# Optimization experiments

Hardware: AMD Instinct MI355X
Metric: run time of the kernel (lower is better)

Reference implementation:

```python
import jax, jax.numpy as jnp
import numpy as np

BZ, C, H, W = 8, 512, 64, 64


def setup_inputs() -> dict:
    key = jax.random.key(0)
    x = jax.random.normal(key, (BZ, C, H, W), dtype=jnp.float32)
    # central square hole: flag==1 -> masked (unknown), flag==0 -> known
    mask = np.zeros((H, W), dtype=np.int32)
    mask[H // 4: 3 * H // 4, W // 4: 3 * W // 4] = 1
    return {"x": x, "mask": jnp.asarray(mask)}


def reference(x, mask):
    # InnerShiftSingle forward with shift_sz=1, stride=1, mask_thred=1:
    # flag == feature-level mask (each 1x1 patch is masked iff its pixel is masked).
    bz, c, h, w = x.shape
    c2 = c // 2
    hw = h * w
    flag = mask.reshape(hw)  # [hw] int, 1=masked, 0=known

    former = x[:, :c2]   # decoder features [b,c2,h,w]
    latter = x[:, c2:]   # encoder features [b,c2,h,w]

    former_f = former.reshape(bz, c2, hw).transpose(0, 2, 1)  # [b,hw,c2]
    latter_f = latter.reshape(bz, c2, hw).transpose(0, 2, 1)  # [b,hw,c2]

    # original: conv of (un-normalized) former with L2-normalized latter 1x1 patches
    latter_n = latter_f / (jnp.linalg.norm(latter_f, axis=-1, keepdims=True) + 1e-8)
    cosine = jnp.einsum('bpc,bqc->bpq', former_f, latter_n)  # [b,hw,hw]
    # only known-region patches (flag==0) are candidate sources
    cosine = jnp.where(flag[None, None, :] == 1, -jnp.inf, cosine)

    best = jnp.argmax(cosine, axis=-1)  # [b,hw] index into known region
    shift = jnp.take_along_axis(latter_f, best[..., None], axis=1)  # [b,hw,c2]
    # only masked positions receive a shifted feature; known positions stay 0
    shift = jnp.where(flag[None, :, None] == 1, shift, jnp.zeros((), x.dtype))
    shift = shift.transpose(0, 2, 1).reshape(bz, c2, h, w)

    return jnp.concatenate([former, latter, shift], axis=1)  # [b, 3c/2, h, w]
```

## Files before the change

### kernel.cpp

```cpp
#include <hip/hip_runtime.h>
#include <math.h>

#define BZc 8
#define Cc 512
#define C2c 256
#define HWc 4096
#define OUTC 768
#define NP 1024
#define NQ 3072
#define QG 8
#define TAU 5e-5f
#define FIXSLOTS 64

typedef _Float16 h8 __attribute__((ext_vector_type(8)));
typedef float f16v __attribute__((ext_vector_type(16)));
typedef float f32x4 __attribute__((ext_vector_type(4)));

__global__ __launch_bounds__(1024) void k_build(const int* __restrict__ mask,
                                                int* __restrict__ pidx,
                                                int* __restrict__ qidx,
                                                int* __restrict__ qinv,
                                                int* __restrict__ cnt) {
    __shared__ int s0[1024], s1[1024], t0[1024], t1[1024];
    int t = threadIdx.x;
    if (t < 8) cnt[t] = 0;
    int f[4];
    int cp = 0;
#pragma unroll
    for (int j = 0; j < 4; ++j) { f[j] = mask[t * 4 + j]; cp += f[j]; }
    s0[t] = cp; s1[t] = 4 - cp;
    __syncthreads();
    int *a = s0, *b = s1, *c = t0, *d = t1;
    for (int off = 1; off < 1024; off <<= 1) {
        int vp = a[t] + (t >= off ? a[t - off] : 0);
        int vq = b[t] + (t >= off ? b[t - off] : 0);
        c[t] = vp; d[t] = vq;
        __syncthreads();
        int* tmp;
        tmp = a; a = c; c = tmp;
        tmp = b; b = d; d = tmp;
    }
    int ep = a[t] - cp;
    int eq = b[t] - (4 - cp);
#pragma unroll
    for (int j = 0; j < 4; ++j) {
        int idx = t * 4 + j;
        if (f[j]) { pidx[ep] = idx; qinv[idx] = -1; ep++; }
        else      { qidx[eq] = idx; qinv[idx] = eq; eq++; }
    }
}

__global__ __launch_bounds__(256) void k_prep(const float* __restrict__ x,
                                              const int* __restrict__ pidx,
                                              const int* __restrict__ qinv,
                                              _Float16* __restrict__ latH,
                                              _Float16* __restrict__ latL,
                                              _Float16* __restrict__ forH,
                                              _Float16* __restrict__ forL,
                                              float* __restrict__ invn,
                                              float* __restrict__ nrm) {
    int id = blockIdx.x;
    bool isLat = id < 512;
    int b  = isLat ? (id >> 6) : ((id - 512) >> 4);
    int bx = isLat ? (id & 63) : ((id - 512) & 15);
    int tid = threadIdx.x;
    __shared__ float tile[64][65];
    __shared__ float sqa[4][64];
    __shared__ float sinv[64];
    __shared__ int rowm[64];
    __shared__ int rowsrc[64];
    if (tid < 64) {
        if (isLat) { int q = bx * 64 + tid; rowsrc[tid] = q; rowm[tid] = qinv[q]; }
        else       { int pc = bx * 64 + tid; rowsrc[tid] = pidx[pc]; rowm[tid] = pc; }
    }
    __syncthreads();
    const float* xb = x + (size_t)b * Cc * HWc + (isLat ? (size_t)C2c * HWc : 0);
    if (isLat) {
        float sacc = 0.f;
        for (int c0 = 0; c0 < 256; c0 += 64) {
            for (int it = 0; it < 16; ++it) {
                int i = tid + it * 256; int cc = i >> 6, qq = i & 63;
                float v = xb[(size_t)(c0 + cc) * HWc + rowsrc[qq]];
                sacc += v * v;
            }
        }
        sqa[tid >> 6][tid & 63] = sacc;
        __syncthreads();
        if (tid < 64) {
            float s = sqa[0][tid] + sqa[1][tid] + sqa[2][tid] + sqa[3][tid];
            float nr = sqrtf(s) + 1e-8f;
            float inv = 1.0f / nr;
            int q = bx * 64 + tid;
            invn[b * HWc + q] = inv; nrm[b * HWc + q] = nr;
            sinv[tid] = inv;
        }
        __syncthreads();
    }
    _Float16* dH = isLat ? latH + (size_t)b * NQ * 256 : forH + (size_t)b * NP * 256;
    _Float16* dL = isLat ? latL + (size_t)b * NQ * 256 : forL + (size_t)b * NP * 256;
    for (int c0 = 0; c0 < 256; c0 += 64) {
        for (int it = 0; it < 16; ++it) {
            int i = tid + it * 256; int cc = i >> 6, qq = i & 63;
            tile[qq][cc] = xb[(size_t)(c0 + cc) * HWc + rowsrc[qq]];
        }
        __syncthreads();
        int qq = tid >> 2, sub = tid & 3;
        int dr = rowm[qq];
        if (dr >= 0) {
            float scale = isLat ? sinv[qq] : 1.0f;
            h8 hv0, hv1, lv0, lv1;
#pragma unroll
            for (int j = 0; j < 8; ++j) {
                float v = tile[qq][sub * 16 + j] * scale;
                _Float16 h = (_Float16)v;
                hv0[j] = h; lv0[j] = (_Float16)((v - (float)h) * 2048.0f);
            }
#pragma unroll
            for (int j = 0; j < 8; ++j) {
                float v = tile[qq][sub * 16 + 8 + j] * scale;
                _Float16 h = (_Float16)v;
                hv1[j] = h; lv1[j] = (_Float16)((v - (float)h) * 2048.0f);
            }
            size_t o = (size_t)dr * 256 + c0 + sub * 16;
            *(h8*)(dH + o) = hv0; *(h8*)(dH + o + 8) = hv1;
            *(h8*)(dL + o) = lv0; *(h8*)(dL + o + 8) = lv1;
        }
        __syncthreads();
    }
}

__global__ __launch_bounds__(512, 2) void k_gemm(const _Float16* __restrict__ latH,
                                                 const _Float16* __restrict__ latL,
                                                 const _Float16* __restrict__ forH,
                                                 const _Float16* __restrict__ forL,
                                                 float* __restrict__ bv1,
                                                 int* __restrict__ bi1,
                                                 float* __restrict__ bv2) {
    int pg = blockIdx.x;
    int qg = blockIdx.y;
    int b  = blockIdx.z;
    int tid = threadIdx.x;
    int w = tid >> 6, lane = tid & 63;
    int l31 = lane & 31, lh = lane >> 5;

    __shared__ __align__(16) _Float16 sH[2][32 * 256];
    __shared__ __align__(16) _Float16 sL[2][32 * 256];

    size_t fo = ((size_t)(b * NP + pg * 256 + w * 32 + l31)) * 256 + lh * 8;
    const _Float16* fH = forH + fo;
    const _Float16* fL = forL + fo;
    h8 BH[16], BL[16];
#pragma unroll
    for (int ks = 0; ks < 16; ++ks) {
        BH[ks] = *(const h8*)(fH + ks * 16);
        BL[ks] = *(const h8*)(fL + ks * 16);
    }

    const _Float16* latHb = latH + (size_t)(b * NQ + qg * 384) * 256;
    const _Float16* latLb = latL + (size_t)(b * NQ + qg * 384) * 256;
    int sq0 = tid >> 5;
    int sq1 = 16 + (tid >> 5);
    int ssl = tid & 31;

    float v1 = -INFINITY, v2 = -INFINITY; int i1 = 0;

    f32x4 rH0, rH1, rL0, rL1;
#define LOADQ(t)                                                                   \
    rH0 = *(const f32x4*)(latHb + ((size_t)((t) * 32 + sq0) * 256 + ssl * 8));     \
    rH1 = *(const f32x4*)(latHb + ((size_t)((t) * 32 + sq1) * 256 + ssl * 8));     \
    rL0 = *(const f32x4*)(latLb + ((size_t)((t) * 32 + sq0) * 256 + ssl * 8));     \
    rL1 = *(const f32x4*)(latLb + ((size_t)((t) * 32 + sq1) * 256 + ssl * 8));
#define WRITEQ(bf)                                                                 \
    *(f32x4*)(&sH[bf][sq0 * 256 + ((ssl ^ sq0) * 8)]) = rH0;                       \
    *(f32x4*)(&sH[bf][sq1 * 256 + ((ssl ^ sq1) * 8)]) = rH1;                       \
    *(f32x4*)(&sL[bf][sq0 * 256 + ((ssl ^ sq0) * 8)]) = rL0;                       \
    *(f32x4*)(&sL[bf][sq1 * 256 + ((ssl ^ sq1) * 8)]) = rL1;

    LOADQ(0); WRITEQ(0);
    __syncthreads();

    for (int t = 0; t < 12; ++t) {
        if (t < 11) { LOADQ(t + 1); }
        const _Float16* bufH = &sH[t & 1][0];
        const _Float16* bufL = &sL[t & 1][0];
        f16v accA = {}, accB = {};
#pragma unroll
        for (int ks = 0; ks < 16; ++ks) {
            int slotA = (ks * 2 + lh) ^ l31;
            h8 aH = *(const h8*)(bufH + l31 * 256 + slotA * 8);
            h8 aL = *(const h8*)(bufL + l31 * 256 + slotA * 8);
            accA = __builtin_amdgcn_mfma_f32_32x32x16_f16(aH, BH[ks], accA, 0, 0, 0);
            accB = __builtin_amdgcn_mfma_f32_32x32x16_f16(aH, BL[ks], accB, 0, 0, 0);
            accB = __builtin_amdgcn_mfma_f32_32x32x16_f16(aL, BH[ks], accB, 0, 0, 0);
        }
        int q0 = qg * 384 + t * 32;
#pragma unroll
        for (int r = 0; r < 16; ++r) {
            float v = accA[r] + accB[r] * (1.0f / 2048.0f);
            int q = q0 + (r & 3) + 8 * (r >> 2) + 4 * lh;
            if (v > v1) { v2 = v1; v1 = v; i1 = q; }
            else if (v > v2) { v2 = v; }
        }
        if (t < 11) { WRITEQ((t + 1) & 1); }
        __syncthreads();
    }
#undef LOADQ
#undef WRITEQ
    float ov1 = __shfl_xor(v1, 32);
    int   oi1 = __shfl_xor(i1, 32);
    float ov2 = __shfl_xor(v2, 32);
    if (ov1 > v1) { v2 = fmaxf(v1, ov2); v1 = ov1; i1 = oi1; }
    else          { v2 = fmaxf(ov1, v2); }
    if (lane < 32) {
        size_t o = ((size_t)b * NP + pg * 256 + w * 32 + lane) * QG + qg;
        bv1[o] = v1; bi1[o] = i1; bv2[o] = v2;
    }
}

__global__ void k_reduce(const float* __restrict__ bv1, const int* __restrict__ bi1,
                         const float* __restrict__ bv2, int* __restrict__ bfin,
                         int* __restrict__ cnt, int* __restrict__ fixrows) {
    int t = blockIdx.x * blockDim.x + threadIdx.x;
    if (t >= BZc * NP) return;
    float V1 = -INFINITY, V2 = -INFINITY; int I1 = 0;
    for (int c = 0; c < QG; ++c) {
        float a = bv1[(size_t)t * QG + c];
        float a2 = bv2[(size_t)t * QG + c];
        int   i = bi1[(size_t)t * QG + c];
        if (a > V1) { V2 = fmaxf(V1, a2); V1 = a; I1 = i; }
        else        { V2 = fmaxf(V2, a); }
    }
    bfin[t] = I1;
    if (V1 - V2 < TAU) {
        int b = t >> 10;
        int s = atomicAdd(&cnt[b], 1);
        if (s < FIXSLOTS) fixrows[b * FIXSLOTS + s] = t & 1023;
    }
}

__global__ __launch_bounds__(256) void k_fixA(const float* __restrict__ x,
                                              const int* __restrict__ pidx,
                                              const int* __restrict__ mask,
                                              const float* __restrict__ invn,
                                              const int* __restrict__ cnt,
                                              const int* __restrict__ fixrows,
                                              float* __restrict__ fixv,
                                              int* __restrict__ fixi) {
    int qg = blockIdx.x, s = blockIdx.y, b = blockIdx.z;
    int n = cnt[b]; if (n > FIXSLOTS) n = FIXSLOTS;
    if (s >= n) return;
    int p = fixrows[b * FIXSLOTS + s];
    int porig = pidx[p];
    int tid = threadIdx.x;
    __shared__ float fs[256];
    fs[tid] = x[((size_t)b * Cc + tid) * HWc + porig];
    __syncthreads();
    const float* lx = x + ((size_t)b * Cc + C2c) * HWc;
    int q0 = qg * 1024 + tid * 4;
    float4 acc = make_float4(0.f, 0.f, 0.f, 0.f);
    for (int c0 = 0; c0 < 256; c0 += 8) {
        float4 v[8];
#pragma unroll
        for (int u = 0; u < 8; ++u)
            v[u] = *(const float4*)(lx + (size_t)(c0 + u) * HWc + q0);
#pragma unroll
        for (int u = 0; u < 8; ++u) {
            float fc = fs[c0 + u];
            acc.x = fmaf(fc, v[u].x, acc.x);
            acc.y = fmaf(fc, v[u].y, acc.y);
            acc.z = fmaf(fc, v[u].z, acc.z);
            acc.w = fmaf(fc, v[u].w, acc.w);
        }
    }
    float vals[4] = {acc.x, acc.y, acc.z, acc.w};
    float bv = -INFINITY; int bq = 1 << 30;
#pragma unroll
    for (int k = 0; k < 4; ++k) {
        int q = q0 + k;
        float val = vals[k] * invn[b * HWc + q];
        if (mask[q] == 0 && val > bv) { bv = val; bq = q; }
    }
    __shared__ float rv[256]; __shared__ int rq[256];
    rv[tid] = bv; rq[tid] = bq; __syncthreads();
    for (int off = 128; off > 0; off >>= 1) {
        if (tid < off) {
            float v2 = rv[tid + off]; int q2 = rq[tid + off];
            if (v2 > rv[tid] || (v2 == rv[tid] && q2 < rq[tid])) { rv[tid] = v2; rq[tid] = q2; }
        }
        __syncthreads();
    }
    if (tid == 0) {
        fixv[(b * FIXSLOTS + s) * 4 + qg] = rv[0];
        fixi[(b * FIXSLOTS + s) * 4 + qg] = rq[0];
    }
}

__global__ void k_fixB(const int* __restrict__ cnt, const int* __restrict__ fixrows,
                       const float* __restrict__ fixv, const int* __restrict__ fixi,
                       const int* __restrict__ qinv, int* __restrict__ bfin) {
    int t = threadIdx.x;
    int b = t >> 6, s = t & 63;
    int n = cnt[b]; if (n > FIXSLOTS) n = FIXSLOTS;
    if (s >= n) return;
    float bv = -INFINITY; int bq = 1 << 30;
    for (int qg = 0; qg < 4; ++qg) {
        float v = fixv[(b * FIXSLOTS + s) * 4 + qg];
        int   q = fixi[(b * FIXSLOTS + s) * 4 + qg];
        if (v > bv || (v == bv && q < bq)) { bv = v; bq = q; }
    }
    int p = fixrows[b * FIXSLOTS + s];
    bfin[b * NP + p] = qinv[bq];
}

__global__ __launch_bounds__(256) void k_fill(const float* __restrict__ x,
                                              float* __restrict__ out) {
    size_t i4 = (size_t)blockIdx.x * blockDim.x + threadIdx.x;
    size_t total4 = (size_t)BZc * OUTC * HWc / 4;
    if (i4 >= total4) return;
    size_t e   = i4 * 4;
    size_t per = (size_t)OUTC * HWc;
    size_t b   = e / per;
    size_t rem = e % per;
    int ch = (int)(rem / HWc);
    float4* o4 = (float4*)out;
    if (ch < Cc) {
        const float4* x4 = (const float4*)x;
        o4[i4] = x4[((size_t)b * Cc * HWc + rem) >> 2];
    } else {
        o4[i4] = make_float4(0.f, 0.f, 0.f, 0.f);
    }
}

__global__ __launch_bounds__(256) void k_scatter(const _Float16* __restrict__ latH,
                                                 const _Float16* __restrict__ latL,
                                                 const float* __restrict__ nrm,
                                                 const int* __restrict__ bfin,
                                                 const int* __restrict__ pidx,
                                                 const int* __restrict__ qidx,
                                                 float* __restrict__ out) {
    int blk = blockIdx.x;
    int b   = blockIdx.y;
    int tid = threadIdx.x;
    __shared__ float tile[32][257];
    __shared__ int qd[32], pd[32];
    __shared__ float nr[32];
    if (tid < 32) {
        int qc = bfin[b * NP + blk * 32 + tid];
        qd[tid] = qc;
        pd[tid] = pidx[blk * 32 + tid];
        nr[tid] = nrm[b * HWc + qidx[qc]];
    }
    __syncthreads();
    for (int i = tid; i < 32 * 256; i += 256) {
        int pp = i >> 8, c = i & 255;
        size_t o = ((size_t)b * NQ + qd[pp]) * 256 + c;
        tile[pp][c] = ((float)latH[o] + (float)latL[o] * (1.0f / 2048.0f)) * nr[pp];
    }
    __syncthreads();
    float* ob = out + (size_t)b * OUTC * HWc + (size_t)Cc * HWc;
    for (int i = tid; i < 256 * 32; i += 256) {
        int ch = i >> 5, j = i & 31;
        ob[(size_t)ch * HWc + pd[j]] = tile[j][ch];
    }
}

extern "C" void kernel_launch(void* const* d_in, const int* in_sizes, int n_in,
                              void* d_out, int out_size, void* d_ws, size_t ws_size,
                              hipStream_t stream) {
    const float* x    = (const float*)d_in[0];
    const int*   mask = (const int*)d_in[1];
    float* out = (float*)d_out;
    char*  ws  = (char*)d_ws;

    _Float16* latH = (_Float16*)(ws);
    _Float16* latL = (_Float16*)(ws + 12582912);
    _Float16* forH = (_Float16*)(ws + 25165824);
    _Float16* forL = (_Float16*)(ws + 29360128);
    float* invn    = (float*)(ws + 33554432);
    float* nrm     = (float*)(ws + 33685504);
    float* bv1     = (float*)(ws + 33816576);
    int*   bi1     = (int*)  (ws + 34078720);
    float* bv2     = (float*)(ws + 34340864);
    int*   bfin    = (int*)  (ws + 34603008);
    int*   pidx    = (int*)  (ws + 34635776);
    int*   qidx    = (int*)  (ws + 34639872);
    int*   qinv    = (int*)  (ws + 34652160);
    int*   cnt     = (int*)  (ws + 34668544);
    int*   fixrows = (int*)  (ws + 34668576);
    float* fixv    = (float*)(ws + 34670624);
    int*   fixi    = (int*)  (ws + 34678816);

    k_build<<<1, 1024, 0, stream>>>(mask, pidx, qidx, qinv, cnt);
    k_prep<<<640, 256, 0, stream>>>(x, pidx, qinv, latH, latL, forH, forL, invn, nrm);
    k_fill<<<(int)(((size_t)BZc * OUTC * HWc / 4 + 255) / 256), 256, 0, stream>>>(x, out);
    k_gemm<<<dim3(4, QG, BZc), 512, 0, stream>>>(latH, latL, forH, forL, bv1, bi1, bv2);
    k_reduce<<<(BZc * NP + 255) / 256, 256, 0, stream>>>(bv1, bi1, bv2, bfin, cnt, fixrows);
    k_fixA<<<dim3(4, FIXSLOTS, BZc), 256, 0, stream>>>(x, pidx, mask, invn, cnt, fixrows, fixv, fixi);
    k_fixB<<<1, 512, 0, stream>>>(cnt, fixrows, fixv, fixi, qinv, bfin);
    k_scatter<<<dim3(32, BZc), 256, 0, stream>>>(latH, latL, nrm, bfin, pidx, qidx, out);
}
```

Measured before the change: 132.2 us.

## Fuse output copy and zero-fill into prep; apply inverse norm in GEMM epilogue

The separate k_fill pass is removed. k_prep now reads x once with contiguous spatial rows, writes the former and latter channels straight to the output, and zeroes the shift channels. Latent features are stored unnormalized, and the per-candidate inverse norm is applied in the GEMM epilogue from shared memory. The scatter therefore no longer rescales by the norm, and the separate norm pass over the latent channels disappears. The trade-off is that prep now runs over all 64-column groups, including masked rows for latent and known rows for former, and it does extra output writes. Precision also shifts slightly, because the fp16 hi/lo split now carries the raw values rather than normalized ones.

```diff
diff --git a/kernel.cpp b/kernel.cpp
--- a/kernel.cpp
+++ b/kernel.cpp
@@ -18,8 +18,8 @@
 
 __global__ __launch_bounds__(1024) void k_build(const int* __restrict__ mask,
                                                 int* __restrict__ pidx,
-                                                int* __restrict__ qidx,
                                                 int* __restrict__ qinv,
+                                                int* __restrict__ pinv,
                                                 int* __restrict__ cnt) {
     __shared__ int s0[1024], s1[1024], t0[1024], t1[1024];
     int t = threadIdx.x;
@@ -45,79 +45,58 @@
 #pragma unroll
     for (int j = 0; j < 4; ++j) {
         int idx = t * 4 + j;
-        if (f[j]) { pidx[ep] = idx; qinv[idx] = -1; ep++; }
-        else      { qidx[eq] = idx; qinv[idx] = eq; eq++; }
+        if (f[j]) { pidx[ep] = idx; pinv[idx] = ep; qinv[idx] = -1; ep++; }
+        else      { qinv[idx] = eq; pinv[idx] = -1; eq++; }
     }
 }
 
 __global__ __launch_bounds__(256) void k_prep(const float* __restrict__ x,
-                                              const int* __restrict__ pidx,
+                                              const int* __restrict__ pinv,
                                               const int* __restrict__ qinv,
                                               _Float16* __restrict__ latH,
                                               _Float16* __restrict__ latL,
                                               _Float16* __restrict__ forH,
                                               _Float16* __restrict__ forL,
                                               float* __restrict__ invn,
-                                              float* __restrict__ nrm) {
+                                              float* __restrict__ invnC,
+                                              float* __restrict__ out) {
     int id = blockIdx.x;
     bool isLat = id < 512;
-    int b  = isLat ? (id >> 6) : ((id - 512) >> 4);
-    int bx = isLat ? (id & 63) : ((id - 512) & 15);
+    int b = isLat ? (id >> 6) : ((id - 512) >> 6);
+    int g = isLat ? (id & 63) : ((id - 512) & 63);
     int tid = threadIdx.x;
     __shared__ float tile[64][65];
     __shared__ float sqa[4][64];
-    __shared__ float sinv[64];
     __shared__ int rowm[64];
-    __shared__ int rowsrc[64];
-    if (tid < 64) {
-        if (isLat) { int q = bx * 64 + tid; rowsrc[tid] = q; rowm[tid] = qinv[q]; }
-        else       { int pc = bx * 64 + tid; rowsrc[tid] = pidx[pc]; rowm[tid] = pc; }
-    }
+    if (tid < 64) rowm[tid] = isLat ? qinv[g * 64 + tid] : pinv[g * 64 + tid];
     __syncthreads();
     const float* xb = x + (size_t)b * Cc * HWc + (isLat ? (size_t)C2c * HWc : 0);
-    if (isLat) {
-        float sacc = 0.f;
-        for (int c0 = 0; c0 < 256; c0 += 64) {
-            for (int it = 0; it < 16; ++it) {
-                int i = tid + it * 256; int cc = i >> 6, qq = i & 63;
-                float v = xb[(size_t)(c0 + cc) * HWc + rowsrc[qq]];
-                sacc += v * v;
-            }
-        }
-        sqa[tid >> 6][tid & 63] = sacc;
-        __syncthreads();
-        if (tid < 64) {
-            float s = sqa[0][tid] + sqa[1][tid] + sqa[2][tid] + sqa[3][tid];
-            float nr = sqrtf(s) + 1e-8f;
-            float inv = 1.0f / nr;
-            int q = bx * 64 + tid;
-            invn[b * HWc + q] = inv; nrm[b * HWc + q] = nr;
-            sinv[tid] = inv;
-        }
-        __syncthreads();
-    }
+    float* ob = out + (size_t)b * OUTC * HWc + (isLat ? (size_t)C2c * HWc : 0);
     _Float16* dH = isLat ? latH + (size_t)b * NQ * 256 : forH + (size_t)b * NP * 256;
     _Float16* dL = isLat ? latL + (size_t)b * NQ * 256 : forL + (size_t)b * NP * 256;
+    float sacc = 0.f;
     for (int c0 = 0; c0 < 256; c0 += 64) {
         for (int it = 0; it < 16; ++it) {
             int i = tid + it * 256; int cc = i >> 6, qq = i & 63;
-            tile[qq][cc] = xb[(size_t)(c0 + cc) * HWc + rowsrc[qq]];
+            float v = xb[(size_t)(c0 + cc) * HWc + g * 64 + qq];
+            tile[qq][cc] = v;
+            ob[(size_t)(c0 + cc) * HWc + g * 64 + qq] = v;
+            sacc += v * v;
         }
         __syncthreads();
         int qq = tid >> 2, sub = tid & 3;
         int dr = rowm[qq];
         if (dr >= 0) {
-            float scale = isLat ? sinv[qq] : 1.0f;
             h8 hv0, hv1, lv0, lv1;
 #pragma unroll
             for (int j = 0; j < 8; ++j) {
-                float v = tile[qq][sub * 16 + j] * scale;
+                float v = tile[qq][sub * 16 + j];
                 _Float16 h = (_Float16)v;
                 hv0[j] = h; lv0[j] = (_Float16)((v - (float)h) * 2048.0f);
             }
 #pragma unroll
             for (int j = 0; j < 8; ++j) {
-                float v = tile[qq][sub * 16 + 8 + j] * scale;
+                float v = tile[qq][sub * 16 + 8 + j];
                 _Float16 h = (_Float16)v;
                 hv1[j] = h; lv1[j] = (_Float16)((v - (float)h) * 2048.0f);
             }
@@ -127,12 +106,32 @@
         }
         __syncthreads();
     }
+    if (isLat) {
+        sqa[tid >> 6][tid & 63] = sacc;
+        __syncthreads();
+        if (tid < 64) {
+            float s = sqa[0][tid] + sqa[1][tid] + sqa[2][tid] + sqa[3][tid];
+            float inv = 1.0f / (sqrtf(s) + 1e-8f);
+            int q = g * 64 + tid;
+            invn[b * HWc + q] = inv;
+            int qc = rowm[tid];
+            if (qc >= 0) invnC[b * NQ + qc] = inv;
+        }
+    } else {
+        float4 z = make_float4(0.f, 0.f, 0.f, 0.f);
+        float* sb = out + (size_t)b * OUTC * HWc + (size_t)Cc * HWc;
+        for (int i = tid; i < 256 * 16; i += 256) {
+            int ch = i >> 4, j4 = i & 15;
+            *(float4*)(sb + (size_t)ch * HWc + g * 64 + j4 * 4) = z;
+        }
+    }
 }
 
 __global__ __launch_bounds__(512, 2) void k_gemm(const _Float16* __restrict__ latH,
                                                  const _Float16* __restrict__ latL,
                                                  const _Float16* __restrict__ forH,
                                                  const _Float16* __restrict__ forL,
+                                                 const float* __restrict__ invnC,
                                                  float* __restrict__ bv1,
                                                  int* __restrict__ bi1,
                                                  float* __restrict__ bv2) {
@@ -145,6 +144,9 @@
 
     __shared__ __align__(16) _Float16 sH[2][32 * 256];
     __shared__ __align__(16) _Float16 sL[2][32 * 256];
+    __shared__ float sInv[384];
+
+    if (tid < 384) sInv[tid] = invnC[b * NQ + qg * 384 + tid];
 
     size_t fo = ((size_t)(b * NP + pg * 256 + w * 32 + l31)) * 256 + lh * 8;
     const _Float16* fH = forH + fo;
@@ -193,11 +195,11 @@
             accB = __builtin_amdgcn_mfma_f32_32x32x16_f16(aH, BL[ks], accB, 0, 0, 0);
             accB = __builtin_amdgcn_mfma_f32_32x32x16_f16(aL, BH[ks], accB, 0, 0, 0);
         }
-        int q0 = qg * 384 + t * 32;
 #pragma unroll
         for (int r = 0; r < 16; ++r) {
-            float v = accA[r] + accB[r] * (1.0f / 2048.0f);
-            int q = q0 + (r & 3) + 8 * (r >> 2) + 4 * lh;
+            int off = (r & 3) + 8 * (r >> 2) + 4 * lh;
+            float v = (accA[r] + accB[r] * (1.0f / 2048.0f)) * sInv[t * 32 + off];
+            int q = qg * 384 + t * 32 + off;
             if (v > v1) { v2 = v1; v1 = v; i1 = q; }
             else if (v > v2) { v2 = v; }
         }
@@ -312,49 +314,25 @@
     bfin[b * NP + p] = qinv[bq];
 }
 
-__global__ __launch_bounds__(256) void k_fill(const float* __restrict__ x,
-                                              float* __restrict__ out) {
-    size_t i4 = (size_t)blockIdx.x * blockDim.x + threadIdx.x;
-    size_t total4 = (size_t)BZc * OUTC * HWc / 4;
-    if (i4 >= total4) return;
-    size_t e   = i4 * 4;
-    size_t per = (size_t)OUTC * HWc;
-    size_t b   = e / per;
-    size_t rem = e % per;
-    int ch = (int)(rem / HWc);
-    float4* o4 = (float4*)out;
-    if (ch < Cc) {
-        const float4* x4 = (const float4*)x;
-        o4[i4] = x4[((size_t)b * Cc * HWc + rem) >> 2];
-    } else {
-        o4[i4] = make_float4(0.f, 0.f, 0.f, 0.f);
-    }
-}
-
 __global__ __launch_bounds__(256) void k_scatter(const _Float16* __restrict__ latH,
                                                  const _Float16* __restrict__ latL,
-                                                 const float* __restrict__ nrm,
                                                  const int* __restrict__ bfin,
                                                  const int* __restrict__ pidx,
-                                                 const int* __restrict__ qidx,
                                                  float* __restrict__ out) {
     int blk = blockIdx.x;
     int b   = blockIdx.y;
     int tid = threadIdx.x;
     __shared__ float tile[32][257];
     __shared__ int qd[32], pd[32];
-    __shared__ float nr[32];
     if (tid < 32) {
-        int qc = bfin[b * NP + blk * 32 + tid];
-        qd[tid] = qc;
+        qd[tid] = bfin[b * NP + blk * 32 + tid];
         pd[tid] = pidx[blk * 32 + tid];
-        nr[tid] = nrm[b * HWc + qidx[qc]];
     }
     __syncthreads();
     for (int i = tid; i < 32 * 256; i += 256) {
         int pp = i >> 8, c = i & 255;
         size_t o = ((size_t)b * NQ + qd[pp]) * 256 + c;
-        tile[pp][c] = ((float)latH[o] + (float)latL[o] * (1.0f / 2048.0f)) * nr[pp];
+        tile[pp][c] = (float)latH[o] + (float)latL[o] * (1.0f / 2048.0f);
     }
     __syncthreads();
     float* ob = out + (size_t)b * OUTC * HWc + (size_t)Cc * HWc;
@@ -377,25 +355,24 @@
     _Float16* forH = (_Float16*)(ws + 25165824);
     _Float16* forL = (_Float16*)(ws + 29360128);
     float* invn    = (float*)(ws + 33554432);
-    float* nrm     = (float*)(ws + 33685504);
-    float* bv1     = (float*)(ws + 33816576);
-    int*   bi1     = (int*)  (ws + 34078720);
-    float* bv2     = (float*)(ws + 34340864);
-    int*   bfin    = (int*)  (ws + 34603008);
-    int*   pidx    = (int*)  (ws + 34635776);
-    int*   qidx    = (int*)  (ws + 34639872);
-    int*   qinv    = (int*)  (ws + 34652160);
-    int*   cnt     = (int*)  (ws + 34668544);
-    int*   fixrows = (int*)  (ws + 34668576);
-    float* fixv    = (float*)(ws + 34670624);
-    int*   fixi    = (int*)  (ws + 34678816);
-
-    k_build<<<1, 1024, 0, stream>>>(mask, pidx, qidx, qinv, cnt);
-    k_prep<<<640, 256, 0, stream>>>(x, pidx, qinv, latH, latL, forH, forL, invn, nrm);
-    k_fill<<<(int)(((size_t)BZc * OUTC * HWc / 4 + 255) / 256), 256, 0, stream>>>(x, out);
-    k_gemm<<<dim3(4, QG, BZc), 512, 0, stream>>>(latH, latL, forH, forL, bv1, bi1, bv2);
+    float* invnC   = (float*)(ws + 33685504);
+    float* bv1     = (float*)(ws + 33783808);
+    int*   bi1     = (int*)  (ws + 34045952);
+    float* bv2     = (float*)(ws + 34308096);
+    int*   bfin    = (int*)  (ws + 34570240);
+    int*   pidx    = (int*)  (ws + 34603008);
+    int*   qinv    = (int*)  (ws + 34607104);
+    int*   pinv    = (int*)  (ws + 34623488);
+    int*   cnt     = (int*)  (ws + 34639872);
+    int*   fixrows = (int*)  (ws + 34639904);
+    float* fixv    = (float*)(ws + 34641952);
+    int*   fixi    = (int*)  (ws + 34650144);
+
+    k_build<<<1, 1024, 0, stream>>>(mask, pidx, qinv, pinv, cnt);
+    k_prep<<<1024, 256, 0, stream>>>(x, pinv, qinv, latH, latL, forH, forL, invn, invnC, out);
+    k_gemm<<<dim3(4, QG, BZc), 512, 0, stream>>>(latH, latL, forH, forL, invnC, bv1, bi1, bv2);
     k_reduce<<<(BZc * NP + 255) / 256, 256, 0, stream>>>(bv1, bi1, bv2, bfin, cnt, fixrows);
     k_fixA<<<dim3(4, FIXSLOTS, BZc), 256, 0, stream>>>(x, pidx, mask, invn, cnt, fixrows, fixv, fixi);
     k_fixB<<<1, 512, 0, stream>>>(cnt, fixrows, fixv, fixi, qinv, bfin);
-    k_scatter<<<dim3(32, BZc), 256, 0, stream>>>(latH, latL, nrm, bfin, pidx, qidx, out);
-}
+    k_scatter<<<dim3(32, BZc), 256, 0, stream>>>(latH, latL, bfin, pidx, out);
+}
```

Result: faster. 120.7 us (-8.7%).
